# Performance work log

Hardware: AMD Instinct MI355X
Metric: run time of the kernel (lower is better)

Reference implementation:

```python
import jax, jax.numpy as jnp
import numpy as np

D = 768
H = 12
EPS = 1e-5


def layer_norm(x, g, b):
    mu = jnp.mean(x, axis=-1, keepdims=True)
    var = jnp.var(x, axis=-1, keepdims=True)
    return (x - mu) * jax.lax.rsqrt(var + EPS) * g + b


def setup_inputs() -> dict:
    key = jax.random.key(0)
    ks = jax.random.split(key, 12)
    d, h = D, H
    x = jax.random.normal(ks[0], (4, 1024, d), dtype=jnp.float32)
    # attention projections (per-head dim is full d, per the module)
    s_qkv = (6.0 / (d + d * h)) ** 0.5  # xavier-like scale
    Wq = jax.random.uniform(ks[1], (d, d * h), jnp.float32, -s_qkv, s_qkv)
    Wk = jax.random.uniform(ks[2], (d, d * h), jnp.float32, -s_qkv, s_qkv)
    Wv = jax.random.uniform(ks[3], (d, d * h), jnp.float32, -s_qkv, s_qkv)
    Wu = jax.random.uniform(ks[4], (d * h, d), jnp.float32, -s_qkv, s_qkv)
    bu = jnp.zeros((d,), jnp.float32)
    # MLP
    s1 = (6.0 / (d + 4 * d)) ** 0.5
    W1 = jax.random.uniform(ks[5], (d, 4 * d), jnp.float32, -s1, s1)
    b1 = jax.random.normal(ks[6], (4 * d,), jnp.float32) * 1e-6
    W2 = jax.random.uniform(ks[7], (4 * d, d), jnp.float32, -s1, s1)
    b2 = jax.random.normal(ks[8], (d,), jnp.float32) * 1e-6
    ln1_g = jnp.ones((d,), jnp.float32)
    ln1_b = jnp.zeros((d,), jnp.float32)
    ln2_g = jnp.ones((d,), jnp.float32)
    ln2_b = jnp.zeros((d,), jnp.float32)
    return dict(x=x, Wq=Wq, Wk=Wk, Wv=Wv, Wu=Wu, bu=bu,
                ln1_g=ln1_g, ln1_b=ln1_b, ln2_g=ln2_g, ln2_b=ln2_b,
                W1=W1, b1=b1, W2=W2, b2=b2)


def reference(x, Wq, Wk, Wv, Wu, bu, ln1_g, ln1_b, ln2_g, ln2_b, W1, b1, W2, b2):
    b, n, d = x.shape
    h = H
    # --- pre-LN attention block ---
    res = x
    y = layer_norm(x, ln1_g, ln1_b)
    qs = (y @ Wq).reshape(b, n, h, d)  # per-head dim = d (module quirk)
    ks = (y @ Wk).reshape(b, n, h, d)
    vs = (y @ Wv).reshape(b, n, h, d)
    scores = jnp.einsum('bihd,bjhd->bhij', qs, ks) / (d ** 0.5)
    w = jax.nn.softmax(scores, axis=-1)
    att = jnp.einsum('bhij,bjhd->bihd', w, vs).reshape(b, n, h * d)
    y = att @ Wu + bu
    x = y + res
    # --- pre-LN MLP block (dropout is identity at inference) ---
    res = x
    y = layer_norm(x, ln2_g, ln2_b)
    y = jax.nn.relu(y @ W1 + b1)
    y = y @ W2 + b2
    return y + res
```

## Files before the change

kernel.cpp:

```cpp
#include <hip/hip_runtime.h>
#include <cstdint>
#include <cmath>


typedef __bf16 bf16_t;
typedef __bf16 bf16x8 __attribute__((ext_vector_type(8)));
typedef __bf16 bf16x4 __attribute__((ext_vector_type(4)));
typedef float floatx4 __attribute__((ext_vector_type(4)));

#define DMODEL 768
#define NHEAD  12
#define SEQ    1024
#define NBATCH 4
#define ROWS   (NBATCH*SEQ)
#define DH     (DMODEL*NHEAD)
#define DFF    (4*DMODEL)

__device__ __forceinline__ void gload16(const bf16_t* g, bf16_t* l)
{
  __builtin_amdgcn_global_load_lds(
      (const __attribute__((address_space(1))) void*)g,
      (__attribute__((address_space(3))) void*)l,
      16, 0, 0);
}

template<bool BIAS, bool RES, bool RELU, int OMODE>
__global__ __launch_bounds__(256)
void gemm_v8(const bf16_t* __restrict__ A, const bf16_t* __restrict__ BT,
             void* __restrict__ Cv, int K, int lda, int ldb, int ldc,
             int bdiv, long sa_hi, long sa_lo, long sb_hi, long sb_lo,
             long sc_hi, long sc_lo,
             const float* __restrict__ bias, const float* __restrict__ res,
             int ldres, float alpha)
{
  __shared__ __align__(16) bf16_t As[128*64];
  __shared__ __align__(16) bf16_t Bs[128*64];

  const long nwg  = (long)gridDim.x * gridDim.y * gridDim.z;
  const long orig = blockIdx.x + (long)gridDim.x * (blockIdx.y + (long)gridDim.y * blockIdx.z);
  const long q8 = nwg >> 3, r8 = nwg & 7;
  const long xcd = orig & 7, loc = orig >> 3;
  const long swz = (xcd < r8 ? xcd*(q8+1) : r8*(q8+1) + (xcd - r8)*q8) + loc;
  const int  bix = (int)(swz % (long)gridDim.x);
  const long rem = swz / (long)gridDim.x;
  const int  biy = (int)(rem % (long)gridDim.y);
  const int  biz = (int)(rem / (long)gridDim.y);

  const int tid  = threadIdx.x;
  const int wave = tid >> 6;
  const int lane = tid & 63;
  const int r    = lane & 15;
  const int q    = lane >> 4;

  A  += (long)(biz / bdiv) * sa_hi + (long)(biz % bdiv) * sa_lo;
  BT += (long)(biz / bdiv) * sb_hi + (long)(biz % bdiv) * sb_lo;
  const long coff = (long)(biz / bdiv) * sc_hi + (long)(biz % bdiv) * sc_lo;

  const int bm = biy * 128;
  const int bn = bix * 128;
  const int wm = (wave & 1) * 64;
  const int wn = (wave >> 1) * 64;
// ... 30 lines not shown
      for (int t = 0; t < 4; ++t) {
        afrag[t] = *(const bf16x8*)(As + p*4096 + (am + t)*512 + lane*8);
        bfrag[t] = *(const bf16x8*)(Bs + p*4096 + (bb + t)*512 + lane*8);
      }
#pragma unroll
      for (int mt = 0; mt < 4; ++mt)
#pragma unroll
        for (int nt = 0; nt < 4; ++nt)
          acc[mt][nt] = __builtin_amdgcn_mfma_f32_16x16x32_bf16(
              afrag[mt], bfrag[nt], acc[mt][nt], 0, 0, 0);
    }
    __syncthreads();
  }

  const int row0 = bm + wm + q*4;
  const int col0 = bn + wn + r;
#pragma unroll
  for (int nt = 0; nt < 4; ++nt) {
    const int col = col0 + nt*16;
    float bv = 0.f;
    if (BIAS) bv = bias[col];
#pragma unroll
    for (int mt = 0; mt < 4; ++mt) {
#pragma unroll
      for (int e = 0; e < 4; ++e) {
        const int rowi = row0 + mt*16 + e;
        float v = acc[mt][nt][e] * alpha;
        if (BIAS) v += bv;
        if (RELU) v = fmaxf(v, 0.f);
        if (RES)  v += res[(long)rowi * ldres + col];
        const long idx = coff + (long)rowi * ldc + col;
        if (OMODE == 0)      ((bf16_t*)Cv)[idx] = (bf16_t)v;
        else if (OMODE == 1) ((float*)Cv)[idx] = v;
        else                 ((float*)Cv)[idx] += v;
      }
    }
  }
}

__global__ void tr_f2b_v8(const float* __restrict__ in, bf16_t* __restrict__ out,
                          int ldi, int ldo)
{
  __shared__ bf16_t tile[32][34];
  const int c0 = blockIdx.x * 32, r0 = blockIdx.y * 32;
  const int tx = threadIdx.x, ty = threadIdx.y;
#pragma unroll
  for (int i = 0; i < 4; ++i)
    tile[ty + 8*i][tx] = (bf16_t)in[(long)(r0 + ty + 8*i) * ldi + c0 + tx];
  __syncthreads();
#pragma unroll
  for (int i = 0; i < 4; ++i)
    out[(long)(c0 + ty + 8*i) * ldo + r0 + tx] = tile[tx][ty + 8*i];
}

__global__ void tr_b_v8(const bf16_t* __restrict__ in, bf16_t* __restrict__ out,
                        int ldi, int ldo, int bdiv,
                        long si_hi, long si_lo, long so_hi, long so_lo)
{
  __shared__ bf16_t tile[32][34];
  const int z = blockIdx.z;
  in  += (long)(z / bdiv) * si_hi + (long)(z % bdiv) * si_lo;
  out += (long)(z / bdiv) * so_hi + (long)(z % bdiv) * so_lo;
  const int c0 = blockIdx.x * 32, r0 = blockIdx.y * 32;
  const int tx = threadIdx.x, ty = threadIdx.y;
#pragma unroll
  for (int i = 0; i < 4; ++i)
    tile[ty + 8*i][tx] = in[(long)(r0 + ty + 8*i) * ldi + c0 + tx];
  __syncthreads();
#pragma unroll
  for (int i = 0; i < 4; ++i)
    out[(long)(c0 + ty + 8*i) * ldo + r0 + tx] = tile[tx][ty + 8*i];
}

__global__ void tr_wh_v8(const float* __restrict__ Wq, const float* __restrict__ Wk,
                         const float* __restrict__ Wv, const float* __restrict__ Wu,
                         bf16_t* __restrict__ WhT, bf16_t* __restrict__ WuTh, int h)
{
  __shared__ bf16_t tile[32][34];
  const int z = blockIdx.z;
  const float* in; bf16_t* out; int ldi;
  if (z < 3) {
    const float* W = (z == 0) ? Wq : (z == 1) ? Wk : Wv;
    in  = W + (long)h * DMODEL;
    ldi = DH;
    out = WhT + (long)z * DMODEL * DMODEL;
  } else {
    in  = Wu + (long)h * DMODEL * DMODEL;
    ldi = DMODEL;
    out = WuTh;
  }
  const int c0 = blockIdx.x * 32, r0 = blockIdx.y * 32;
  const int tx = threadIdx.x, ty = threadIdx.y;
#pragma unroll
  for (int i = 0; i < 4; ++i)
    tile[ty + 8*i][tx] = (bf16_t)in[(long)(r0 + ty + 8*i) * ldi + c0 + tx];
  __syncthreads();
#pragma unroll
  for (int i = 0; i < 4; ++i)
    out[(long)(c0 + ty + 8*i) * DMODEL + r0 + tx] = tile[tx][ty + 8*i];
}

__global__ void cast3_v8(const float* __restrict__ a, const float* __restrict__ b,
                         const float* __restrict__ c,
                         bf16_t* __restrict__ oa, bf16_t* __restrict__ ob,
                         bf16_t* __restrict__ oc)
{
  const float* src = (blockIdx.z == 0) ? a : (blockIdx.z == 1) ? b : c;
  bf16_t* dst      = (blockIdx.z == 0) ? oa : (blockIdx.z == 1) ? ob : oc;
  const long i = ((long)blockIdx.x * 256 + threadIdx.x) * 4;
  float4 v = *(const float4*)(src + i);
  bf16x4 o;
  o[0] = (bf16_t)v.x; o[1] = (bf16_t)v.y; o[2] = (bf16_t)v.z; o[3] = (bf16_t)v.w;
  *(bf16x4*)(dst + i) = o;
}

__global__ void cast1_v8(const float* __restrict__ src, bf16_t* __restrict__ dst)
{
  const long i = ((long)blockIdx.x * 256 + threadIdx.x) * 4;
  float4 v = *(const float4*)(src + i);
  bf16x4 o;
  o[0] = (bf16_t)v.x; o[1] = (bf16_t)v.y; o[2] = (bf16_t)v.z; o[3] = (bf16_t)v.w;
  *(bf16x4*)(dst + i) = o;
}

__global__ void ln_v8(const float* __restrict__ x, const float* __restrict__ g,
                      const float* __restrict__ b, bf16_t* __restrict__ y)
{
  const long row = blockIdx.x;
  const int tid = threadIdx.x;
  const float* xr = x + row * DMODEL;
  float v0 = xr[tid], v1 = xr[tid + 256], v2 = xr[tid + 512];
  float s  = v0 + v1 + v2;
  float ss = v0*v0 + v1*v1 + v2*v2;
  for (int o = 32; o; o >>= 1) { s += __shfl_down(s, o); ss += __shfl_down(ss, o); }
  __shared__ float rs[4], rss[4];
  const int wave = tid >> 6, lane = tid & 63;
  if (lane == 0) { rs[wave] = s; rss[wave] = ss; }
  __syncthreads();
  s  = rs[0] + rs[1] + rs[2] + rs[3];
  ss = rss[0] + rss[1] + rss[2] + rss[3];
  const float inv = 1.0f / (float)DMODEL;
  const float mean = s * inv;
  const float var  = ss * inv - mean * mean;
  const float rstd = rsqrtf(var + 1e-5f);
  bf16_t* yr = y + row * DMODEL;
  yr[tid]       = (bf16_t)(((v0 - mean) * rstd) * g[tid]       + b[tid]);
  yr[tid + 256] = (bf16_t)(((v1 - mean) * rstd) * g[tid + 256] + b[tid + 256]);
  yr[tid + 512] = (bf16_t)(((v2 - mean) * rstd) * g[tid + 512] + b[tid + 512]);
}

__global__ void softmax_v8(bf16_t* __restrict__ S)
{
  const long row = blockIdx.x;
  const int tid = threadIdx.x;
  bf16_t* p = S + row * SEQ + tid * 4;
  bf16x4 v = *(const bf16x4*)p;
  float f0 = (float)v[0], f1 = (float)v[1], f2 = (float)v[2], f3 = (float)v[3];
  float m = fmaxf(fmaxf(f0, f1), fmaxf(f2, f3));
  for (int o = 32; o; o >>= 1) m = fmaxf(m, __shfl_down(m, o));
  __shared__ float rm[4], rsum[4];
  const int wave = tid >> 6, lane = tid & 63;
  if (lane == 0) rm[wave] = m;
  __syncthreads();
  m = fmaxf(fmaxf(rm[0], rm[1]), fmaxf(rm[2], rm[3]));
  float e0 = __expf(f0 - m), e1 = __expf(f1 - m), e2 = __expf(f2 - m), e3 = __expf(f3 - m);
  float s = e0 + e1 + e2 + e3;
  for (int o = 32; o; o >>= 1) s += __shfl_down(s, o);
  if (lane == 0) rsum[wave] = s;
  __syncthreads();
  s = rsum[0] + rsum[1] + rsum[2] + rsum[3];
  const float invs = 1.0f / s;
  bf16x4 o4;
  o4[0] = (bf16_t)(e0 * invs); o4[1] = (bf16_t)(e1 * invs);
  o4[2] = (bf16_t)(e2 * invs); o4[3] = (bf16_t)(e3 * invs);
  *(bf16x4*)p = o4;
}

__global__ void finalize_v8(const float* __restrict__ acc, const float* __restrict__ add,
                            const float* __restrict__ bias, float* __restrict__ o)
{
  const long i = (long)blockIdx.x * 256 + threadIdx.x;
  const int c = (int)(i % DMODEL);
  o[i] = acc[i] + bias[c] + add[i];
}

template<int NP>
__global__ void reduce_v8(const float* __restrict__ p, const float* __restrict__ add,
                          const float* __restrict__ bias, float* __restrict__ o,
                          long plane)
{
  const long i = ((long)blockIdx.x * 256 + threadIdx.x) * 4;
  float4 s = *(const float4*)(p + i);
#pragma unroll
  for (int n = 1; n < NP; ++n) {
    float4 v = *(const float4*)(p + i + (long)n * plane);
    s.x += v.x; s.y += v.y; s.z += v.z; s.w += v.w;
  }
  const int c = (int)(i % DMODEL);
  float4 bv = *(const float4*)(bias + c);
  float4 av = *(const float4*)(add + i);
  float4 r;
  r.x = s.x + bv.x + av.x; r.y = s.y + bv.y + av.y;
  r.z = s.z + bv.z + av.z; r.w = s.w + bv.w + av.w;
  *(float4*)(o + i) = r;
}

extern "C" void kernel_launch(void* const* d_in, const int* in_sizes, int n_in,
                              void* d_out, int out_size, void* d_ws, size_t ws_size,
                              hipStream_t stream)
{
  (void)in_sizes; (void)n_in; (void)out_size;
  const float* x    = (const float*)d_in[0];
  const float* Wq   = (const float*)d_in[1];
  const float* Wk   = (const float*)d_in[2];
  const float* Wv   = (const float*)d_in[3];
  const float* Wu   = (const float*)d_in[4];
  const float* bu   = (const float*)d_in[5];
  const float* ln1g = (const float*)d_in[6];
  const float* ln1b = (const float*)d_in[7];
  const float* ln2g = (const float*)d_in[8];
  const float* ln2b = (const float*)d_in[9];
  const float* W1   = (const float*)d_in[10];
  const float* b1   = (const float*)d_in[11];
  const float* W2   = (const float*)d_in[12];
  const float* b2   = (const float*)d_in[13];
  float* out = (float*)d_out;

  char* ws = (char*)d_ws;
  size_t off = 0;
  auto alloc = [&](size_t bytes) -> void* {
    void* p = (void*)(ws + off);
    off += (bytes + 255) & ~(size_t)255;
    return p;
  };

  const float qk_alpha = 1.0f / sqrtf((float)DMODEL);
  dim3 tb(32, 8);

  const size_t SZ_W   = (size_t)DMODEL * DH * 2;
  const size_t SZ_MT  = (size_t)NHEAD * DMODEL * DMODEL * 2;
  const size_t SZ_Y   = (size_t)ROWS * DMODEL * 2;
  const size_t SZ_X2  = (size_t)ROWS * DMODEL * 4;

  if (ws_size >= (size_t)262e6) {
    bf16_t* MT   = (bf16_t*)alloc(SZ_MT);
    bf16_t* PhT  = (bf16_t*)alloc(SZ_MT);
    bf16_t* y    = (bf16_t*)alloc(SZ_Y);
    float*  x2f  = (float* )alloc(SZ_X2);
    float*  part = (float* )alloc((size_t)3 * ROWS * DMODEL * 4);
    bf16_t* S    = (bf16_t*)alloc((size_t)NBATCH * SEQ * NHEAD * SEQ * 2);
    bf16_t* Zt   = (bf16_t*)alloc((size_t)NBATCH * DMODEL * NHEAD * SEQ * 2);
    bf16_t* T2   = (bf16_t*)part;
    bf16_t* Wqb  = (bf16_t*)S;
    bf16_t* Wkb  = (bf16_t*)((char*)S + SZ_W);
    bf16_t* Wvb  = (bf16_t*)((char*)S + 2*SZ_W);
    bf16_t* WuT  = (bf16_t*)((char*)S + 3*SZ_W);
    bf16_t* W1T  = (bf16_t*)S;
    bf16_t* W2T  = (bf16_t*)((char*)S + 4718592);
    bf16_t* t    = (bf16_t*)((char*)S + 9437184);
    float*  partM= (float* )((char*)S + 34603008);
    bf16_t* y2   = (bf16_t*)Zt;

    cast3_v8<<<dim3(6912, 1, 3), 256, 0, stream>>>(Wq, Wk, Wv, Wqb, Wkb, Wvb);
    tr_f2b_v8<<<dim3(DMODEL/32, DH/32), tb, 0, stream>>>(Wu, WuT, DMODEL, DH);
    gemm_v8<false,false,false,0><<<dim3(6, 6, NHEAD), 256, 0, stream>>>(
        Wkb, Wqb, MT, DMODEL, DH, DH, DMODEL, NHEAD,
        0, DMODEL, 0, DMODEL, 0, (long)DMODEL*DMODEL, nullptr, nullptr, 0, 1.0f);
    gemm_v8<false,false,false,0><<<dim3(6, 6, NHEAD), 256, 0, stream>>>(
        WuT, Wvb, PhT, DMODEL, DH, DH, DMODEL, NHEAD,
        0, DMODEL, 0, DMODEL, 0, (long)DMODEL*DMODEL, nullptr, nullptr, 0, 1.0f);

    ln_v8<<<ROWS, 256, 0, stream>>>(x, ln1g, ln1b, y);
    for (int b0 = 0; b0 < NBATCH; b0 += 2) {
      const bf16_t* yb = y + (long)b0 * SEQ * DMODEL;
      gemm_v8<false,false,false,0><<<dim3(6, 8, 2*NHEAD), 256, 0, stream>>>(
          yb, MT, T2, DMODEL, DMODEL, DMODEL, DMODEL, NHEAD,
          (long)SEQ*DMODEL, 0, 0, (long)DMODEL*DMODEL,
          (long)NHEAD*SEQ*DMODEL, (long)SEQ*DMODEL,
          nullptr, nullptr, 0, 1.0f);
      gemm_v8<false,false,false,0><<<dim3(8, 8, 2*NHEAD), 256, 0, stream>>>(
          T2, yb, S + (long)b0*SEQ*NHEAD*SEQ, DMODEL, DMODEL, DMODEL, NHEAD*SEQ, NHEAD,
          (long)NHEAD*SEQ*DMODEL, (long)SEQ*DMODEL,
          (long)SEQ*DMODEL, 0,
          (long)SEQ*NHEAD*SEQ, (long)SEQ,
          nullptr, nullptr, 0, qk_alpha);
    }
    softmax_v8<<<NBATCH*SEQ*NHEAD, 256, 0, stream>>>(S);
    gemm_v8<false,false,false,0><<<dim3(8, 6, NBATCH*NHEAD), 256, 0, stream>>>(
        PhT, y, Zt, DMODEL, DMODEL, DMODEL, NHEAD*SEQ, NHEAD,
        0, (long)DMODEL*DMODEL, (long)SEQ*DMODEL, 0,
        (long)DMODEL*NHEAD*SEQ, (long)SEQ, nullptr, nullptr, 0, 1.0f);
    gemm_v8<false,false,false,1><<<dim3(6, 8, 12), 256, 0, stream>>>(
        S, Zt, part, NHEAD*SEQ/3, NHEAD*SEQ, NHEAD*SEQ, DMODEL, NBATCH,
        (long)(NHEAD*SEQ/3), (long)SEQ*NHEAD*SEQ,
        (long)(NHEAD*SEQ/3), (long)DMODEL*NHEAD*SEQ,
        (long)ROWS*DMODEL, (long)SEQ*DMODEL, nullptr, nullptr, 0, 1.0f);
    reduce_v8<3><<<(ROWS*DMODEL)/1024, 256, 0, stream>>>(
        part, x, bu, x2f, (long)ROWS*DMODEL);

    tr_f2b_v8<<<dim3(DFF/32, DMODEL/32), tb, 0, stream>>>(W1, W1T, DFF, DMODEL);
    tr_f2b_v8<<<dim3(DMODEL/32, DFF/32), tb, 0, stream>>>(W2, W2T, DMODEL, DFF);
    ln_v8<<<ROWS, 256, 0, stream>>>(x2f, ln2g, ln2b, y2);
    gemm_v8<true,false,true,0><<<dim3(DFF/128, ROWS/128, 1), 256, 0, stream>>>(
        y2, W1T, t, DMODEL, DMODEL, DMODEL, DFF, 1, 0,0,0,0,0,0, b1, nullptr, 0, 1.0f);
    gemm_v8<false,false,false,1><<<dim3(6, ROWS/128, 4), 256, 0, stream>>>(
        t, W2T, partM, DFF/4, DFF, DFF, DMODEL, 4,
        0, (long)(DFF/4), 0, (long)(DFF/4), 0, (long)ROWS*DMODEL,
        nullptr, nullptr, 0, 1.0f);
    reduce_v8<4><<<(ROWS*DMODEL)/1024, 256, 0, stream>>>(
        partM, x2f, b2, out, (long)ROWS*DMODEL);
  } else if (ws_size >= (size_t)112e6) {
    bf16_t* MT  = (bf16_t*)alloc(SZ_MT);
    bf16_t* PhT = (bf16_t*)alloc(SZ_MT);
    bf16_t* y   = (bf16_t*)alloc(SZ_Y);
    float*  x2f = (float* )alloc(SZ_X2);
    char*   BIG = (char*  )alloc((size_t)62914560);
    bf16_t* T_b  = (bf16_t*)(BIG);
    bf16_t* S_b  = (bf16_t*)(BIG + 18874368);
    bf16_t* Zt_b = (bf16_t*)(BIG + 44040192);
    float*  part = (float* )(BIG);
    bf16_t* Wqb = (bf16_t*)(BIG);
    bf16_t* Wkb = (bf16_t*)(BIG + SZ_W);
    bf16_t* Wvb = (bf16_t*)(BIG + 2*SZ_W);
    bf16_t* WuT = (bf16_t*)(BIG + 3*SZ_W);
    bf16_t* W1T   = (bf16_t*)(BIG);
    bf16_t* W2T   = (bf16_t*)(BIG + 4718592);
    bf16_t* t     = (bf16_t*)(BIG + 9437184);
    float*  partM = (float* )(BIG + 34603008);
    bf16_t* y2    = y;

    cast3_v8<<<dim3(6912, 1, 3), 256, 0, stream>>>(Wq, Wk, Wv, Wqb, Wkb, Wvb);
    tr_f2b_v8<<<dim3(DMODEL/32, DH/32), tb, 0, stream>>>(Wu, WuT, DMODEL, DH);
    gemm_v8<false,false,false,0><<<dim3(6, 6, NHEAD), 256, 0, stream>>>(
        Wkb, Wqb, MT, DMODEL, DH, DH, DMODEL, NHEAD,
        0, DMODEL, 0, DMODEL, 0, (long)DMODEL*DMODEL, nullptr, nullptr, 0, 1.0f);
    gemm_v8<false,false,false,0><<<dim3(6, 6, NHEAD), 256, 0, stream>>>(
        WuT, Wvb, PhT, DMODEL, DH, DH, DMODEL, NHEAD,
        0, DMODEL, 0, DMODEL, 0, (long)DMODEL*DMODEL, nullptr, nullptr, 0, 1.0f);

    ln_v8<<<ROWS, 256, 0, stream>>>(x, ln1g, ln1b, y);
    for (int b = 0; b < NBATCH; ++b) {
      const bf16_t* yb = y + (long)b * SEQ * DMODEL;
      gemm_v8<false,false,false,0><<<dim3(6, 8, NHEAD), 256, 0, stream>>>(
          yb, MT, T_b, DMODEL, DMODEL, DMODEL, DMODEL, NHEAD,
          0, 0, 0, (long)DMODEL*DMODEL, 0, (long)SEQ*DMODEL,
          nullptr, nullptr, 0, 1.0f);
      gemm_v8<false,false,false,0><<<dim3(8, 8, NHEAD), 256, 0, stream>>>(
          T_b, yb, S_b, DMODEL, DMODEL, DMODEL, NHEAD*SEQ, NHEAD,
          0, (long)SEQ*DMODEL, 0, 0, 0, (long)SEQ,
          nullptr, nullptr, 0, qk_alpha);
      softmax_v8<<<NHEAD*SEQ, 256, 0, stream>>>(S_b);
      gemm_v8<false,false,false,0><<<dim3(8, 6, NHEAD), 256, 0, stream>>>(
          PhT, yb, Zt_b, DMODEL, DMODEL, DMODEL, NHEAD*SEQ, NHEAD,
          0, (long)DMODEL*DMODEL, 0, 0, 0, (long)SEQ,
          nullptr, nullptr, 0, 1.0f);
      gemm_v8<false,false,false,1><<<dim3(6, 8, 6), 256, 0, stream>>>(
          S_b, Zt_b, part, NHEAD*SEQ/6, NHEAD*SEQ, NHEAD*SEQ, DMODEL, 6,
          0, (long)(NHEAD*SEQ/6), 0, (long)(NHEAD*SEQ/6), 0, (long)SEQ*DMODEL,
          nullptr, nullptr, 0, 1.0f);
      reduce_v8<6><<<(SEQ*DMODEL)/1024, 256, 0, stream>>>(
          part, x + (long)b*SEQ*DMODEL, bu, x2f + (long)b*SEQ*DMODEL,
          (long)SEQ*DMODEL);
    }

    tr_f2b_v8<<<dim3(DFF/32, DMODEL/32), tb, 0, stream>>>(W1, W1T, DFF, DMODEL);
    tr_f2b_v8<<<dim3(DMODEL/32, DFF/32), tb, 0, stream>>>(W2, W2T, DMODEL, DFF);
    ln_v8<<<ROWS, 256, 0, stream>>>(x2f, ln2g, ln2b, y2);
    gemm_v8<true,false,true,0><<<dim3(DFF/128, ROWS/128, 1), 256, 0, stream>>>(
        y2, W1T, t, DMODEL, DMODEL, DMODEL, DFF, 1, 0,0,0,0,0,0, b1, nullptr, 0, 1.0f);
    gemm_v8<false,false,false,1><<<dim3(6, ROWS/128, 2), 256, 0, stream>>>(
        t, W2T, partM, DFF/2, DFF, DFF, DMODEL, 2,
        0, (long)(DFF/2), 0, (long)(DFF/2), 0, (long)ROWS*DMODEL,
        nullptr, nullptr, 0, 1.0f);
    reduce_v8<2><<<(ROWS*DMODEL)/1024, 256, 0, stream>>>(
        partM, x2f, b2, out, (long)ROWS*DMODEL);
  } else if (ws_size >= (size_t)70e6) {
    bf16_t* MT  = (bf16_t*)alloc(SZ_MT);
    bf16_t* PhT = (bf16_t*)alloc(SZ_MT);
    bf16_t* y   = (bf16_t*)alloc(SZ_Y);
    char*   R   = (char*  )alloc((size_t)33554432);
    bf16_t* WAb = (bf16_t*)(R);
    bf16_t* WBb = (bf16_t*)(R + SZ_W);
    float*  x2f = (float* )(R);
    bf16_t* T_h = (bf16_t*)(R + 12582912);
    bf16_t* S_h = (bf16_t*)(R + 18874368);
    bf16_t* Z_h = (bf16_t*)(R + 27262976);
    bf16_t* W1T = (bf16_t*)(R + 12582912);
    bf16_t* W2T = (bf16_t*)(R + 17301504);
    bf16_t* t   = (bf16_t*)MT;
    bf16_t* y2  = y;

    cast1_v8<<<6912, 256, 0, stream>>>(Wq, WAb);
    cast1_v8<<<6912, 256, 0, stream>>>(Wk, WBb);
    gemm_v8<false,false,false,0><<<dim3(6, 6, NHEAD), 256, 0, stream>>>(
        WBb, WAb, MT, DMODEL, DH, DH, DMODEL, NHEAD,
        0, DMODEL, 0, DMODEL, 0, (long)DMODEL*DMODEL, nullptr, nullptr, 0, 1.0f);
    cast1_v8<<<6912, 256, 0, stream>>>(Wv, WAb);
    tr_f2b_v8<<<dim3(DMODEL/32, DH/32), tb, 0, stream>>>(Wu, WBb, DMODEL, DH);
    gemm_v8<false,false,false,0><<<dim3(6, 6, NHEAD), 256, 0, stream>>>(
        WBb, WAb, PhT, DMODEL, DH, DH, DMODEL, NHEAD,
        0, DMODEL, 0, DMODEL, 0, (long)DMODEL*DMODEL, nullptr, nullptr, 0, 1.0f);

    ln_v8<<<ROWS, 256, 0, stream>>>(x, ln1g, ln1b, y);
    for (int h = 0; h < NHEAD; ++h) {
      const bf16_t* MTh  = MT  + (long)h * DMODEL * DMODEL;
      const bf16_t* PhTh = PhT + (long)h * DMODEL * DMODEL;
      gemm_v8<false,false,false,0><<<dim3(6, ROWS/128, 1), 256, 0, stream>>>(
          y, MTh, T_h, DMODEL, DMODEL, DMODEL, DMODEL, 1,
          0,0,0,0,0,0, nullptr, nullptr, 0, 1.0f);
      gemm_v8<false,false,false,0><<<dim3(8, 8, NBATCH), 256, 0, stream>>>(
          T_h, y, S_h, DMODEL, DMODEL, DMODEL, SEQ, NBATCH,
          0, (long)SEQ*DMODEL, 0, (long)SEQ*DMODEL, 0, (long)SEQ*SEQ,
          nullptr, nullptr, 0, qk_alpha);
      softmax_v8<<<ROWS, 256, 0, stream>>>(S_h);
      gemm_v8<false,false,false,0><<<dim3(8, 6, NBATCH), 256, 0, stream>>>(
          PhTh, y, Z_h, DMODEL, DMODEL, DMODEL, SEQ, NBATCH,
          0, 0, 0, (long)SEQ*DMODEL, 0, (long)DMODEL*SEQ,
          nullptr, nullptr, 0, 1.0f);
      if (h == 0)
        gemm_v8<false,false,false,1><<<dim3(6, 8, NBATCH), 256, 0, stream>>>(
            S_h, Z_h, x2f, SEQ, SEQ, SEQ, DMODEL, NBATCH,
            0, (long)SEQ*SEQ, 0, (long)DMODEL*SEQ, 0, (long)SEQ*DMODEL,
            nullptr, nullptr, 0, 1.0f);
      else
        gemm_v8<false,false,false,2><<<dim3(6, 8, NBATCH), 256, 0, stream>>>(
            S_h, Z_h, x2f, SEQ, SEQ, SEQ, DMODEL, NBATCH,
            0, (long)SEQ*SEQ, 0, (long)DMODEL*SEQ, 0, (long)SEQ*DMODEL,
            nullptr, nullptr, 0, 1.0f);
    }
    finalize_v8<<<(ROWS*DMODEL)/256, 256, 0, stream>>>(x2f, x, bu, x2f);

    tr_f2b_v8<<<dim3(DFF/32, DMODEL/32), tb, 0, stream>>>(W1, W1T, DFF, DMODEL);
    tr_f2b_v8<<<dim3(DMODEL/32, DFF/32), tb, 0, stream>>>(W2, W2T, DMODEL, DFF);
    ln_v8<<<ROWS, 256, 0, stream>>>(x2f, ln2g, ln2b, y2);
    gemm_v8<true,false,true,0><<<dim3(DFF/128, ROWS/128, 1), 256, 0, stream>>>(
        y2, W1T, t, DMODEL, DMODEL, DMODEL, DFF, 1, 0,0,0,0,0,0, b1, nullptr, 0, 1.0f);
    gemm_v8<true,true,false,1><<<dim3(6, ROWS/128, 1), 256, 0, stream>>>(
        t, W2T, out, DFF/2, DFF, DFF, DMODEL, 1, 0,0,0,0,0,0,
        b2, x2f, DMODEL, 1.0f);
    gemm_v8<false,false,false,2><<<dim3(6, ROWS/128, 1), 256, 0, stream>>>(
        t + DFF/2, W2T + DFF/2, out, DFF/2, DFF, DFF, DMODEL, 1, 0,0,0,0,0,0,
        nullptr, nullptr, 0, 1.0f);
  } else {
    bf16_t* W1T   = (bf16_t*)alloc((size_t)DMODEL * DFF * 2);
    bf16_t* W2T   = (bf16_t*)alloc((size_t)DMODEL * DFF * 2);
    bf16_t* y     = (bf16_t*)alloc(SZ_Y);
    float*  x2f   = (float* )alloc(SZ_X2);
    char*   reg1  = (char*)alloc((size_t)3*DMODEL*DMODEL*2 + (size_t)DMODEL*DMODEL*2 + (size_t)SEQ*DMODEL*2);
    bf16_t* WhT   = (bf16_t*)reg1;
    bf16_t* WuTh  = (bf16_t*)(reg1 + (size_t)3*DMODEL*DMODEL*2);
    bf16_t* attb  = (bf16_t*)(reg1 + (size_t)4*DMODEL*DMODEL*2);
    bf16_t* y2    = (bf16_t*)reg1;
    char*   reg2  = (char*)alloc((size_t)SEQ*3*DMODEL*2 + (size_t)DMODEL*SEQ*2 + (size_t)SEQ*SEQ*2);
    bf16_t* QKVb  = (bf16_t*)reg2;
    bf16_t* Vtb   = (bf16_t*)(reg2 + (size_t)SEQ*3*DMODEL*2);
    bf16_t* Sb    = (bf16_t*)(reg2 + (size_t)SEQ*3*DMODEL*2 + (size_t)DMODEL*SEQ*2);
    bf16_t* tslab = (bf16_t*)reg2;

    tr_f2b_v8<<<dim3(DFF/32, DMODEL/32), tb, 0, stream>>>(W1, W1T, DFF, DMODEL);
    tr_f2b_v8<<<dim3(DMODEL/32, DFF/32), tb, 0, stream>>>(W2, W2T, DMODEL, DFF);
    ln_v8<<<ROWS, 256, 0, stream>>>(x, ln1g, ln1b, y);

    const int N3 = 3 * DMODEL;
    for (int h = 0; h < NHEAD; ++h) {
      tr_wh_v8<<<dim3(24, 24, 4), tb, 0, stream>>>(Wq, Wk, Wv, Wu, WhT, WuTh, h);
      for (int b = 0; b < NBATCH; ++b) {
        const bf16_t* yb = y + (size_t)b * SEQ * DMODEL;
        gemm_v8<false,false,false,0><<<dim3(N3/128, SEQ/128, 1), 256, 0, stream>>>(
            yb, WhT, QKVb, DMODEL, DMODEL, DMODEL, N3, 1, 0,0,0,0,0,0,
            nullptr, nullptr, 0, 1.0f);
        tr_b_v8<<<dim3(DMODEL/32, SEQ/32, 1), tb, 0, stream>>>(
            QKVb + 2*DMODEL, Vtb, N3, SEQ, 1, 0,0,0,0);
        gemm_v8<false,false,false,0><<<dim3(SEQ/128, SEQ/128, 1), 256, 0, stream>>>(
            QKVb, QKVb + DMODEL, Sb, DMODEL, N3, N3, SEQ, 1, 0,0,0,0,0,0,
            nullptr, nullptr, 0, qk_alpha);
        softmax_v8<<<SEQ, 256, 0, stream>>>(Sb);
        gemm_v8<false,false,false,0><<<dim3(DMODEL/128, SEQ/128, 1), 256, 0, stream>>>(
            Sb, Vtb, attb, SEQ, SEQ, SEQ, DMODEL, 1, 0,0,0,0,0,0,
            nullptr, nullptr, 0, 1.0f);
        float* x2b = x2f + (size_t)b * SEQ * DMODEL;
        if (h == 0)
          gemm_v8<false,false,false,1><<<dim3(DMODEL/128, SEQ/128, 1), 256, 0, stream>>>(
              attb, WuTh, x2b, DMODEL, DMODEL, DMODEL, DMODEL, 1, 0,0,0,0,0,0,
              nullptr, nullptr, 0, 1.0f);
        else
          gemm_v8<false,false,false,2><<<dim3(DMODEL/128, SEQ/128, 1), 256, 0, stream>>>(
              attb, WuTh, x2b, DMODEL, DMODEL, DMODEL, DMODEL, 1, 0,0,0,0,0,0,
              nullptr, nullptr, 0, 1.0f);
      }
    }
    finalize_v8<<<(ROWS*DMODEL)/256, 256, 0, stream>>>(x2f, x, bu, x2f);
    ln_v8<<<ROWS, 256, 0, stream>>>(x2f, ln2g, ln2b, y2);
    for (int kb = 0; kb < 4; ++kb) {
      gemm_v8<true,false,true,0><<<dim3(DMODEL/128, ROWS/128, 1), 256, 0, stream>>>(
          y2, W1T + (size_t)kb*DMODEL*DMODEL, tslab, DMODEL, DMODEL, DMODEL, DMODEL, 1,
          0,0,0,0,0,0, b1 + kb*DMODEL, nullptr, 0, 1.0f);
      if (kb == 0)
        gemm_v8<true,true,false,1><<<dim3(DMODEL/128, ROWS/128, 1), 256, 0, stream>>>(
            tslab, W2T + (size_t)kb*DMODEL, out, DMODEL, DMODEL, DFF, DMODEL, 1,
            0,0,0,0,0,0, b2, x2f, DMODEL, 1.0f);
      else
        gemm_v8<false,false,false,2><<<dim3(DMODEL/128, ROWS/128, 1), 256, 0, stream>>>(
            tslab, W2T + (size_t)kb*DMODEL, out, DMODEL, DMODEL, DFF, DMODEL, 1,
            0,0,0,0,0,0, nullptr, nullptr, 0, 1.0f);
    }
  }
}
```

Measured before the change: 994.3 us.

## Replace split-K partial buffers and reductions with atomic-add epilogue, merge batch loop

Adds an atomic-add output mode to the GEMM and uses it for the split-K attention output (now split 8 ways) and the MLP down-projection, with a small init kernel that pre-writes residual plus bias. This removes the partial-sum buffers and the separate reduce kernels, and lowers the workspace threshold for the fast path. The two-iteration batch loop is collapsed into single launches over all batches. Float atomics make the summation order nondeterministic and add contention on the outputs.

```diff
diff --git a/kernel.cpp b/kernel.cpp
--- a/kernel.cpp
+++ b/kernel.cpp
@@ -26,7 +26,7 @@
 
 template<bool BIAS, bool RES, bool RELU, int OMODE>
 __global__ __launch_bounds__(256)
-void gemm_v8(const bf16_t* __restrict__ A, const bf16_t* __restrict__ BT,
+void gemm_v9(const bf16_t* __restrict__ A, const bf16_t* __restrict__ BT,
              void* __restrict__ Cv, int K, int lda, int ldb, int ldc,
              int bdiv, long sa_hi, long sa_lo, long sb_hi, long sb_lo,
              long sc_hi, long sc_lo,
@@ -123,13 +123,14 @@
         const long idx = coff + (long)rowi * ldc + col;
         if (OMODE == 0)      ((bf16_t*)Cv)[idx] = (bf16_t)v;
         else if (OMODE == 1) ((float*)Cv)[idx] = v;
-        else                 ((float*)Cv)[idx] += v;
+        else if (OMODE == 2) ((float*)Cv)[idx] += v;
+        else                 unsafeAtomicAdd(&((float*)Cv)[idx], v);
       }
     }
   }
 }
 
-__global__ void tr_f2b_v8(const float* __restrict__ in, bf16_t* __restrict__ out,
+__global__ void tr_f2b_v9(const float* __restrict__ in, bf16_t* __restrict__ out,
                           int ldi, int ldo)
 {
   __shared__ bf16_t tile[32][34];
@@ -144,7 +145,7 @@
     out[(long)(c0 + ty + 8*i) * ldo + r0 + tx] = tile[tx][ty + 8*i];
 }
 
-__global__ void tr_b_v8(const bf16_t* __restrict__ in, bf16_t* __restrict__ out,
+__global__ void tr_b_v9(const bf16_t* __restrict__ in, bf16_t* __restrict__ out,
                         int ldi, int ldo, int bdiv,
                         long si_hi, long si_lo, long so_hi, long so_lo)
 {
@@ -163,7 +164,7 @@
     out[(long)(c0 + ty + 8*i) * ldo + r0 + tx] = tile[tx][ty + 8*i];
 }
 
-__global__ void tr_wh_v8(const float* __restrict__ Wq, const float* __restrict__ Wk,
+__global__ void tr_wh_v9(const float* __restrict__ Wq, const float* __restrict__ Wk,
                          const float* __restrict__ Wv, const float* __restrict__ Wu,
                          bf16_t* __restrict__ WhT, bf16_t* __restrict__ WuTh, int h)
 {
@@ -191,7 +192,7 @@
     out[(long)(c0 + ty + 8*i) * DMODEL + r0 + tx] = tile[tx][ty + 8*i];
 }
 
-__global__ void cast3_v8(const float* __restrict__ a, const float* __restrict__ b,
+__global__ void cast3_v9(const float* __restrict__ a, const float* __restrict__ b,
                          const float* __restrict__ c,
                          bf16_t* __restrict__ oa, bf16_t* __restrict__ ob,
                          bf16_t* __restrict__ oc)
@@ -205,7 +206,7 @@
   *(bf16x4*)(dst + i) = o;
 }
 
-__global__ void cast1_v8(const float* __restrict__ src, bf16_t* __restrict__ dst)
+__global__ void cast1_v9(const float* __restrict__ src, bf16_t* __restrict__ dst)
 {
   const long i = ((long)blockIdx.x * 256 + threadIdx.x) * 4;
   float4 v = *(const float4*)(src + i);
@@ -214,7 +215,7 @@
   *(bf16x4*)(dst + i) = o;
 }
 
-__global__ void ln_v8(const float* __restrict__ x, const float* __restrict__ g,
+__global__ void ln_v9(const float* __restrict__ x, const float* __restrict__ g,
                       const float* __restrict__ b, bf16_t* __restrict__ y)
 {
   const long row = blockIdx.x;
@@ -240,7 +241,7 @@
   yr[tid + 512] = (bf16_t)(((v2 - mean) * rstd) * g[tid + 512] + b[tid + 512]);
 }
 
-__global__ void softmax_v8(bf16_t* __restrict__ S)
+__global__ void softmax_v9(bf16_t* __restrict__ S)
 {
   const long row = blockIdx.x;
   const int tid = threadIdx.x;
@@ -267,7 +268,7 @@
   *(bf16x4*)p = o4;
 }
 
-__global__ void finalize_v8(const float* __restrict__ acc, const float* __restrict__ add,
+__global__ void finalize_v9(const float* __restrict__ acc, const float* __restrict__ add,
                             const float* __restrict__ bias, float* __restrict__ o)
 {
   const long i = (long)blockIdx.x * 256 + threadIdx.x;
@@ -275,8 +276,20 @@
   o[i] = acc[i] + bias[c] + add[i];
 }
 
+__global__ void initb_v9(const float* __restrict__ add, const float* __restrict__ bias,
+                         float* __restrict__ o)
+{
+  const long i = ((long)blockIdx.x * 256 + threadIdx.x) * 4;
+  const int c = (int)(i % DMODEL);
+  float4 av = *(const float4*)(add + i);
+  float4 bv = *(const float4*)(bias + c);
+  float4 r;
+  r.x = av.x + bv.x; r.y = av.y + bv.y; r.z = av.z + bv.z; r.w = av.w + bv.w;
+  *(float4*)(o + i) = r;
+}
+
 template<int NP>
-__global__ void reduce_v8(const float* __restrict__ p, const float* __restrict__ add,
+__global__ void reduce_v9(const float* __restrict__ p, const float* __restrict__ add,
                           const float* __restrict__ bias, float* __restrict__ o,
                           long plane)
 {
@@ -333,15 +346,14 @@
   const size_t SZ_Y   = (size_t)ROWS * DMODEL * 2;
   const size_t SZ_X2  = (size_t)ROWS * DMODEL * 4;
 
-  if (ws_size >= (size_t)262e6) {
+  if (ws_size >= (size_t)230e6) {
     bf16_t* MT   = (bf16_t*)alloc(SZ_MT);
     bf16_t* PhT  = (bf16_t*)alloc(SZ_MT);
     bf16_t* y    = (bf16_t*)alloc(SZ_Y);
     float*  x2f  = (float* )alloc(SZ_X2);
-    float*  part = (float* )alloc((size_t)3 * ROWS * DMODEL * 4);
     bf16_t* S    = (bf16_t*)alloc((size_t)NBATCH * SEQ * NHEAD * SEQ * 2);
     bf16_t* Zt   = (bf16_t*)alloc((size_t)NBATCH * DMODEL * NHEAD * SEQ * 2);
-    bf16_t* T2   = (bf16_t*)part;
+    bf16_t* T    = (bf16_t*)Zt;
     bf16_t* Wqb  = (bf16_t*)S;
     bf16_t* Wkb  = (bf16_t*)((char*)S + SZ_W);
     bf16_t* Wvb  = (bf16_t*)((char*)S + 2*SZ_W);
@@ -349,57 +361,48 @@
     bf16_t* W1T  = (bf16_t*)S;
     bf16_t* W2T  = (bf16_t*)((char*)S + 4718592);
     bf16_t* t    = (bf16_t*)((char*)S + 9437184);
-    float*  partM= (float* )((char*)S + 34603008);
     bf16_t* y2   = (bf16_t*)Zt;
 
-    cast3_v8<<<dim3(6912, 1, 3), 256, 0, stream>>>(Wq, Wk, Wv, Wqb, Wkb, Wvb);
-    tr_f2b_v8<<<dim3(DMODEL/32, DH/32), tb, 0, stream>>>(Wu, WuT, DMODEL, DH);
-    gemm_v8<false,false,false,0><<<dim3(6, 6, NHEAD), 256, 0, stream>>>(
+    cast3_v9<<<dim3(6912, 1, 3), 256, 0, stream>>>(Wq, Wk, Wv, Wqb, Wkb, Wvb);
+    tr_f2b_v9<<<dim3(DMODEL/32, DH/32), tb, 0, stream>>>(Wu, WuT, DMODEL, DH);
+    gemm_v9<false,false,false,0><<<dim3(6, 6, NHEAD), 256, 0, stream>>>(
         Wkb, Wqb, MT, DMODEL, DH, DH, DMODEL, NHEAD,
         0, DMODEL, 0, DMODEL, 0, (long)DMODEL*DMODEL, nullptr, nullptr, 0, 1.0f);
-    gemm_v8<false,false,false,0><<<dim3(6, 6, NHEAD), 256, 0, stream>>>(
+    gemm_v9<false,false,false,0><<<dim3(6, 6, NHEAD), 256, 0, stream>>>(
         WuT, Wvb, PhT, DMODEL, DH, DH, DMODEL, NHEAD,
         0, DMODEL, 0, DMODEL, 0, (long)DMODEL*DMODEL, nullptr, nullptr, 0, 1.0f);
 
-    ln_v8<<<ROWS, 256, 0, stream>>>(x, ln1g, ln1b, y);
-    for (int b0 = 0; b0 < NBATCH; b0 += 2) {
-      const bf16_t* yb = y + (long)b0 * SEQ * DMODEL;
-      gemm_v8<false,false,false,0><<<dim3(6, 8, 2*NHEAD), 256, 0, stream>>>(
-          yb, MT, T2, DMODEL, DMODEL, DMODEL, DMODEL, NHEAD,
-          (long)SEQ*DMODEL, 0, 0, (long)DMODEL*DMODEL,
-          (long)NHEAD*SEQ*DMODEL, (long)SEQ*DMODEL,
-          nullptr, nullptr, 0, 1.0f);
-      gemm_v8<false,false,false,0><<<dim3(8, 8, 2*NHEAD), 256, 0, stream>>>(
-          T2, yb, S + (long)b0*SEQ*NHEAD*SEQ, DMODEL, DMODEL, DMODEL, NHEAD*SEQ, NHEAD,
-          (long)NHEAD*SEQ*DMODEL, (long)SEQ*DMODEL,
-          (long)SEQ*DMODEL, 0,
-          (long)SEQ*NHEAD*SEQ, (long)SEQ,
-          nullptr, nullptr, 0, qk_alpha);
-    }
-    softmax_v8<<<NBATCH*SEQ*NHEAD, 256, 0, stream>>>(S);
-    gemm_v8<false,false,false,0><<<dim3(8, 6, NBATCH*NHEAD), 256, 0, stream>>>(
+    ln_v9<<<ROWS, 256, 0, stream>>>(x, ln1g, ln1b, y);
+    gemm_v9<false,false,false,0><<<dim3(6, 8, NBATCH*NHEAD), 256, 0, stream>>>(
+        y, MT, T, DMODEL, DMODEL, DMODEL, DMODEL, NHEAD,
+        (long)SEQ*DMODEL, 0, 0, (long)DMODEL*DMODEL,
+        (long)NHEAD*SEQ*DMODEL, (long)SEQ*DMODEL, nullptr, nullptr, 0, 1.0f);
+    gemm_v9<false,false,false,0><<<dim3(8, 8, NBATCH*NHEAD), 256, 0, stream>>>(
+        T, y, S, DMODEL, DMODEL, DMODEL, NHEAD*SEQ, NHEAD,
+        (long)NHEAD*SEQ*DMODEL, (long)SEQ*DMODEL, (long)SEQ*DMODEL, 0,
+        (long)SEQ*NHEAD*SEQ, (long)SEQ, nullptr, nullptr, 0, qk_alpha);
+    softmax_v9<<<NBATCH*SEQ*NHEAD, 256, 0, stream>>>(S);
+    gemm_v9<false,false,false,0><<<dim3(8, 6, NBATCH*NHEAD), 256, 0, stream>>>(
         PhT, y, Zt, DMODEL, DMODEL, DMODEL, NHEAD*SEQ, NHEAD,
         0, (long)DMODEL*DMODEL, (long)SEQ*DMODEL, 0,
         (long)DMODEL*NHEAD*SEQ, (long)SEQ, nullptr, nullptr, 0, 1.0f);
-    gemm_v8<false,false,false,1><<<dim3(6, 8, 12), 256, 0, stream>>>(
-        S, Zt, part, NHEAD*SEQ/3, NHEAD*SEQ, NHEAD*SEQ, DMODEL, NBATCH,
-        (long)(NHEAD*SEQ/3), (long)SEQ*NHEAD*SEQ,
-        (long)(NHEAD*SEQ/3), (long)DMODEL*NHEAD*SEQ,
-        (long)ROWS*DMODEL, (long)SEQ*DMODEL, nullptr, nullptr, 0, 1.0f);
-    reduce_v8<3><<<(ROWS*DMODEL)/1024, 256, 0, stream>>>(
-        part, x, bu, x2f, (long)ROWS*DMODEL);
-
-    tr_f2b_v8<<<dim3(DFF/32, DMODEL/32), tb, 0, stream>>>(W1, W1T, DFF, DMODEL);
-    tr_f2b_v8<<<dim3(DMODEL/32, DFF/32), tb, 0, stream>>>(W2, W2T, DMODEL, DFF);
-    ln_v8<<<ROWS, 256, 0, stream>>>(x2f, ln2g, ln2b, y2);
-    gemm_v8<true,false,true,0><<<dim3(DFF/128, ROWS/128, 1), 256, 0, stream>>>(
+    initb_v9<<<(ROWS*DMODEL)/1024, 256, 0, stream>>>(x, bu, x2f);
+    gemm_v9<false,false,false,3><<<dim3(6, 8, 32), 256, 0, stream>>>(
+        S, Zt, x2f, NHEAD*SEQ/8, NHEAD*SEQ, NHEAD*SEQ, DMODEL, NBATCH,
+        (long)(NHEAD*SEQ/8), (long)SEQ*NHEAD*SEQ,
+        (long)(NHEAD*SEQ/8), (long)DMODEL*NHEAD*SEQ,
+        0, (long)SEQ*DMODEL, nullptr, nullptr, 0, 1.0f);
+
+    ln_v9<<<ROWS, 256, 0, stream>>>(x2f, ln2g, ln2b, y2);
+    tr_f2b_v9<<<dim3(DFF/32, DMODEL/32), tb, 0, stream>>>(W1, W1T, DFF, DMODEL);
+    tr_f2b_v9<<<dim3(DMODEL/32, DFF/32), tb, 0, stream>>>(W2, W2T, DMODEL, DFF);
+    gemm_v9<true,false,true,0><<<dim3(DFF/128, ROWS/128, 1), 256, 0, stream>>>(
         y2, W1T, t, DMODEL, DMODEL, DMODEL, DFF, 1, 0,0,0,0,0,0, b1, nullptr, 0, 1.0f);
-    gemm_v8<false,false,false,1><<<dim3(6, ROWS/128, 4), 256, 0, stream>>>(
-        t, W2T, partM, DFF/4, DFF, DFF, DMODEL, 4,
-        0, (long)(DFF/4), 0, (long)(DFF/4), 0, (long)ROWS*DMODEL,
+    initb_v9<<<(ROWS*DMODEL)/1024, 256, 0, stream>>>(x2f, b2, out);
+    gemm_v9<false,false,false,3><<<dim3(6, ROWS/128, 4), 256, 0, stream>>>(
+        t, W2T, out, DFF/4, DFF, DFF, DMODEL, 4,
+        0, (long)(DFF/4), 0, (long)(DFF/4), 0, 0,
         nullptr, nullptr, 0, 1.0f);
-    reduce_v8<4><<<(ROWS*DMODEL)/1024, 256, 0, stream>>>(
-        partM, x2f, b2, out, (long)ROWS*DMODEL);
   } else if (ws_size >= (size_t)112e6) {
     bf16_t* MT  = (bf16_t*)alloc(SZ_MT);
     bf16_t* PhT = (bf16_t*)alloc(SZ_MT);
@@ -420,50 +423,50 @@
     float*  partM = (float* )(BIG + 34603008);
     bf16_t* y2    = y;
 
-    cast3_v8<<<dim3(6912, 1, 3), 256, 0, stream>>>(Wq, Wk, Wv, Wqb, Wkb, Wvb);
-    tr_f2b_v8<<<dim3(DMODEL/32, DH/32), tb, 0, stream>>>(Wu, WuT, DMODEL, DH);
-    gemm_v8<false,false,false,0><<<dim3(6, 6, NHEAD), 256, 0, stream>>>(
+    cast3_v9<<<dim3(6912, 1, 3), 256, 0, stream>>>(Wq, Wk, Wv, Wqb, Wkb, Wvb);
+    tr_f2b_v9<<<dim3(DMODEL/32, DH/32), tb, 0, stream>>>(Wu, WuT, DMODEL, DH);
+    gemm_v9<false,false,false,0><<<dim3(6, 6, NHEAD), 256, 0, stream>>>(
         Wkb, Wqb, MT, DMODEL, DH, DH, DMODEL, NHEAD,
         0, DMODEL, 0, DMODEL, 0, (long)DMODEL*DMODEL, nullptr, nullptr, 0, 1.0f);
-    gemm_v8<false,false,false,0><<<dim3(6, 6, NHEAD), 256, 0, stream>>>(
+    gemm_v9<false,false,false,0><<<dim3(6, 6, NHEAD), 256, 0, stream>>>(
         WuT, Wvb, PhT, DMODEL, DH, DH, DMODEL, NHEAD,
         0, DMODEL, 0, DMODEL, 0, (long)DMODEL*DMODEL, nullptr, nullptr, 0, 1.0f);
 
-    ln_v8<<<ROWS, 256, 0, stream>>>(x, ln1g, ln1b, y);
+    ln_v9<<<ROWS, 256, 0, stream>>>(x, ln1g, ln1b, y);
     for (int b = 0; b < NBATCH; ++b) {
       const bf16_t* yb = y + (long)b * SEQ * DMODEL;
-      gemm_v8<false,false,false,0><<<dim3(6, 8, NHEAD), 256, 0, stream>>>(
+      gemm_v9<false,false,false,0><<<dim3(6, 8, NHEAD), 256, 0, stream>>>(
           yb, MT, T_b, DMODEL, DMODEL, DMODEL, DMODEL, NHEAD,
           0, 0, 0, (long)DMODEL*DMODEL, 0, (long)SEQ*DMODEL,
           nullptr, nullptr, 0, 1.0f);
-      gemm_v8<false,false,false,0><<<dim3(8, 8, NHEAD), 256, 0, stream>>>(
+      gemm_v9<false,false,false,0><<<dim3(8, 8, NHEAD), 256, 0, stream>>>(
           T_b, yb, S_b, DMODEL, DMODEL, DMODEL, NHEAD*SEQ, NHEAD,
           0, (long)SEQ*DMODEL, 0, 0, 0, (long)SEQ,
           nullptr, nullptr, 0, qk_alpha);
-      softmax_v8<<<NHEAD*SEQ, 256, 0, stream>>>(S_b);
-      gemm_v8<false,false,false,0><<<dim3(8, 6, NHEAD), 256, 0, stream>>>(
+      softmax_v9<<<NHEAD*SEQ, 256, 0, stream>>>(S_b);
+      gemm_v9<false,false,false,0><<<dim3(8, 6, NHEAD), 256, 0, stream>>>(
           PhT, yb, Zt_b, DMODEL, DMODEL, DMODEL, NHEAD*SEQ, NHEAD,
           0, (long)DMODEL*DMODEL, 0, 0, 0, (long)SEQ,
           nullptr, nullptr, 0, 1.0f);
-      gemm_v8<false,false,false,1><<<dim3(6, 8, 6), 256, 0, stream>>>(
+      gemm_v9<false,false,false,1><<<dim3(6, 8, 6), 256, 0, stream>>>(
           S_b, Zt_b, part, NHEAD*SEQ/6, NHEAD*SEQ, NHEAD*SEQ, DMODEL, 6,
           0, (long)(NHEAD*SEQ/6), 0, (long)(NHEAD*SEQ/6), 0, (long)SEQ*DMODEL,
           nullptr, nullptr, 0, 1.0f);
-      reduce_v8<6><<<(SEQ*DMODEL)/1024, 256, 0, stream>>>(
+      reduce_v9<6><<<(SEQ*DMODEL)/1024, 256, 0, stream>>>(
           part, x + (long)b*SEQ*DMODEL, bu, x2f + (long)b*SEQ*DMODEL,
           (long)SEQ*DMODEL);
     }
 
-    tr_f2b_v8<<<dim3(DFF/32, DMODEL/32), tb, 0, stream>>>(W1, W1T, DFF, DMODEL);
-    tr_f2b_v8<<<dim3(DMODEL/32, DFF/32), tb, 0, stream>>>(W2, W2T, DMODEL, DFF);
-    ln_v8<<<ROWS, 256, 0, stream>>>(x2f, ln2g, ln2b, y2);
-    gemm_v8<true,false,true,0><<<dim3(DFF/128, ROWS/128, 1), 256, 0, stream>>>(
+    tr_f2b_v9<<<dim3(DFF/32, DMODEL/32), tb, 0, stream>>>(W1, W1T, DFF, DMODEL);
+    tr_f2b_v9<<<dim3(DMODEL/32, DFF/32), tb, 0, stream>>>(W2, W2T, DMODEL, DFF);
+    ln_v9<<<ROWS, 256, 0, stream>>>(x2f, ln2g, ln2b, y2);
+    gemm_v9<true,false,true,0><<<dim3(DFF/128, ROWS/128, 1), 256, 0, stream>>>(
         y2, W1T, t, DMODEL, DMODEL, DMODEL, DFF, 1, 0,0,0,0,0,0, b1, nullptr, 0, 1.0f);
-    gemm_v8<false,false,false,1><<<dim3(6, ROWS/128, 2), 256, 0, stream>>>(
+    gemm_v9<false,false,false,1><<<dim3(6, ROWS/128, 2), 256, 0, stream>>>(
         t, W2T, partM, DFF/2, DFF, DFF, DMODEL, 2,
         0, (long)(DFF/2), 0, (long)(DFF/2), 0, (long)ROWS*DMODEL,
         nullptr, nullptr, 0, 1.0f);
-    reduce_v8<2><<<(ROWS*DMODEL)/1024, 256, 0, stream>>>(
+    reduce_v9<2><<<(ROWS*DMODEL)/1024, 256, 0, stream>>>(
         partM, x2f, b2, out, (long)ROWS*DMODEL);
   } else if (ws_size >= (size_t)70e6) {
     bf16_t* MT  = (bf16_t*)alloc(SZ_MT);
@@ -481,55 +484,55 @@
     bf16_t* t   = (bf16_t*)MT;
     bf16_t* y2  = y;
 
-    cast1_v8<<<6912, 256, 0, stream>>>(Wq, WAb);
-    cast1_v8<<<6912, 256, 0, stream>>>(Wk, WBb);
-    gemm_v8<false,false,false,0><<<dim3(6, 6, NHEAD), 256, 0, stream>>>(
+    cast1_v9<<<6912, 256, 0, stream>>>(Wq, WAb);
+    cast1_v9<<<6912, 256, 0, stream>>>(Wk, WBb);
+    gemm_v9<false,false,false,0><<<dim3(6, 6, NHEAD), 256, 0, stream>>>(
         WBb, WAb, MT, DMODEL, DH, DH, DMODEL, NHEAD,
         0, DMODEL, 0, DMODEL, 0, (long)DMODEL*DMODEL, nullptr, nullptr, 0, 1.0f);
-    cast1_v8<<<6912, 256, 0, stream>>>(Wv, WAb);
-    tr_f2b_v8<<<dim3(DMODEL/32, DH/32), tb, 0, stream>>>(Wu, WBb, DMODEL, DH);
-    gemm_v8<false,false,false,0><<<dim3(6, 6, NHEAD), 256, 0, stream>>>(
+    cast1_v9<<<6912, 256, 0, stream>>>(Wv, WAb);
+    tr_f2b_v9<<<dim3(DMODEL/32, DH/32), tb, 0, stream>>>(Wu, WBb, DMODEL, DH);
+    gemm_v9<false,false,false,0><<<dim3(6, 6, NHEAD), 256, 0, stream>>>(
         WBb, WAb, PhT, DMODEL, DH, DH, DMODEL, NHEAD,
         0, DMODEL, 0, DMODEL, 0, (long)DMODEL*DMODEL, nullptr, nullptr, 0, 1.0f);
 
-    ln_v8<<<ROWS, 256, 0, stream>>>(x, ln1g, ln1b, y);
+    ln_v9<<<ROWS, 256, 0, stream>>>(x, ln1g, ln1b, y);
     for (int h = 0; h < NHEAD; ++h) {
       const bf16_t* MTh  = MT  + (long)h * DMODEL * DMODEL;
       const bf16_t* PhTh = PhT + (long)h * DMODEL * DMODEL;
-      gemm_v8<false,false,false,0><<<dim3(6, ROWS/128, 1), 256, 0, stream>>>(
+      gemm_v9<false,false,false,0><<<dim3(6, ROWS/128, 1), 256, 0, stream>>>(
           y, MTh, T_h, DMODEL, DMODEL, DMODEL, DMODEL, 1,
           0,0,0,0,0,0, nullptr, nullptr, 0, 1.0f);
-      gemm_v8<false,false,false,0><<<dim3(8, 8, NBATCH), 256, 0, stream>>>(
+      gemm_v9<false,false,false,0><<<dim3(8, 8, NBATCH), 256, 0, stream>>>(
           T_h, y, S_h, DMODEL, DMODEL, DMODEL, SEQ, NBATCH,
           0, (long)SEQ*DMODEL, 0, (long)SEQ*DMODEL, 0, (long)SEQ*SEQ,
           nullptr, nullptr, 0, qk_alpha);
-      softmax_v8<<<ROWS, 256, 0, stream>>>(S_h);
-      gemm_v8<false,false,false,0><<<dim3(8, 6, NBATCH), 256, 0, stream>>>(
+      softmax_v9<<<ROWS, 256, 0, stream>>>(S_h);
+      gemm_v9<false,false,false,0><<<dim3(8, 6, NBATCH), 256, 0, stream>>>(
           PhTh, y, Z_h, DMODEL, DMODEL, DMODEL, SEQ, NBATCH,
           0, 0, 0, (long)SEQ*DMODEL, 0, (long)DMODEL*SEQ,
           nullptr, nullptr, 0, 1.0f);
       if (h == 0)
-        gemm_v8<false,false,false,1><<<dim3(6, 8, NBATCH), 256, 0, stream>>>(
+        gemm_v9<false,false,false,1><<<dim3(6, 8, NBATCH), 256, 0, stream>>>(
             S_h, Z_h, x2f, SEQ, SEQ, SEQ, DMODEL, NBATCH,
             0, (long)SEQ*SEQ, 0, (long)DMODEL*SEQ, 0, (long)SEQ*DMODEL,
             nullptr, nullptr, 0, 1.0f);
       else
-        gemm_v8<false,false,false,2><<<dim3(6, 8, NBATCH), 256, 0, stream>>>(
+        gemm_v9<false,false,false,2><<<dim3(6, 8, NBATCH), 256, 0, stream>>>(
             S_h, Z_h, x2f, SEQ, SEQ, SEQ, DMODEL, NBATCH,
             0, (long)SEQ*SEQ, 0, (long)DMODEL*SEQ, 0, (long)SEQ*DMODEL,
             nullptr, nullptr, 0, 1.0f);
     }
-    finalize_v8<<<(ROWS*DMODEL)/256, 256, 0, stream>>>(x2f, x, bu, x2f);
-
-    tr_f2b_v8<<<dim3(DFF/32, DMODEL/32), tb, 0, stream>>>(W1, W1T, DFF, DMODEL);
-    tr_f2b_v8<<<dim3(DMODEL/32, DFF/32), tb, 0, stream>>>(W2, W2T, DMODEL, DFF);
-    ln_v8<<<ROWS, 256, 0, stream>>>(x2f, ln2g, ln2b, y2);
-    gemm_v8<true,false,true,0><<<dim3(DFF/128, ROWS/128, 1), 256, 0, stream>>>(
+    finalize_v9<<<(ROWS*DMODEL)/256, 256, 0, stream>>>(x2f, x, bu, x2f);
+
+    tr_f2b_v9<<<dim3(DFF/32, DMODEL/32), tb, 0, stream>>>(W1, W1T, DFF, DMODEL);
+    tr_f2b_v9<<<dim3(DMODEL/32, DFF/32), tb, 0, stream>>>(W2, W2T, DMODEL, DFF);
+    ln_v9<<<ROWS, 256, 0, stream>>>(x2f, ln2g, ln2b, y2);
+    gemm_v9<true,false,true,0><<<dim3(DFF/128, ROWS/128, 1), 256, 0, stream>>>(
         y2, W1T, t, DMODEL, DMODEL, DMODEL, DFF, 1, 0,0,0,0,0,0, b1, nullptr, 0, 1.0f);
-    gemm_v8<true,true,false,1><<<dim3(6, ROWS/128, 1), 256, 0, stream>>>(
+    gemm_v9<true,true,false,1><<<dim3(6, ROWS/128, 1), 256, 0, stream>>>(
         t, W2T, out, DFF/2, DFF, DFF, DMODEL, 1, 0,0,0,0,0,0,
         b2, x2f, DMODEL, 1.0f);
-    gemm_v8<false,false,false,2><<<dim3(6, ROWS/128, 1), 256, 0, stream>>>(
+    gemm_v9<false,false,false,2><<<dim3(6, ROWS/128, 1), 256, 0, stream>>>(
         t + DFF/2, W2T + DFF/2, out, DFF/2, DFF, DFF, DMODEL, 1, 0,0,0,0,0,0,
         nullptr, nullptr, 0, 1.0f);
   } else {
@@ -548,50 +551,50 @@
     bf16_t* Sb    = (bf16_t*)(reg2 + (size_t)SEQ*3*DMODEL*2 + (size_t)DMODEL*SEQ*2);
     bf16_t* tslab = (bf16_t*)reg2;
 
-    tr_f2b_v8<<<dim3(DFF/32, DMODEL/32), tb, 0, stream>>>(W1, W1T, DFF, DMODEL);
-    tr_f2b_v8<<<dim3(DMODEL/32, DFF/32), tb, 0, stream>>>(W2, W2T, DMODEL, DFF);
-    ln_v8<<<ROWS, 256, 0, stream>>>(x, ln1g, ln1b, y);
+    tr_f2b_v9<<<dim3(DFF/32, DMODEL/32), tb, 0, stream>>>(W1, W1T, DFF, DMODEL);
+    tr_f2b_v9<<<dim3(DMODEL/32, DFF/32), tb, 0, stream>>>(W2, W2T, DMODEL, DFF);
+    ln_v9<<<ROWS, 256, 0, stream>>>(x, ln1g, ln1b, y);
 
     const int N3 = 3 * DMODEL;
     for (int h = 0; h < NHEAD; ++h) {
-      tr_wh_v8<<<dim3(24, 24, 4), tb, 0, stream>>>(Wq, Wk, Wv, Wu, WhT, WuTh, h);
+      tr_wh_v9<<<dim3(24, 24, 4), tb, 0, stream>>>(Wq, Wk, Wv, Wu, WhT, WuTh, h);
       for (int b = 0; b < NBATCH; ++b) {
         const bf16_t* yb = y + (size_t)b * SEQ * DMODEL;
-        gemm_v8<false,false,false,0><<<dim3(N3/128, SEQ/128, 1), 256, 0, stream>>>(
+        gemm_v9<false,false,false,0><<<dim3(N3/128, SEQ/128, 1), 256, 0, stream>>>(
             yb, WhT, QKVb, DMODEL, DMODEL, DMODEL, N3, 1, 0,0,0,0,0,0,
             nullptr, nullptr, 0, 1.0f);
-        tr_b_v8<<<dim3(DMODEL/32, SEQ/32, 1), tb, 0, stream>>>(
+        tr_b_v9<<<dim3(DMODEL/32, SEQ/32, 1), tb, 0, stream>>>(
             QKVb + 2*DMODEL, Vtb, N3, SEQ, 1, 0,0,0,0);
-        gemm_v8<false,false,false,0><<<dim3(SEQ/128, SEQ/128, 1), 256, 0, stream>>>(
+        gemm_v9<false,false,false,0><<<dim3(SEQ/128, SEQ/128, 1), 256, 0, stream>>>(
             QKVb, QKVb + DMODEL, Sb, DMODEL, N3, N3, SEQ, 1, 0,0,0,0,0,0,
             nullptr, nullptr, 0, qk_alpha);
-        softmax_v8<<<SEQ, 256, 0, stream>>>(Sb);
-        gemm_v8<false,false,false,0><<<dim3(DMODEL/128, SEQ/128, 1), 256, 0, stream>>>(
+        softmax_v9<<<SEQ, 256, 0, stream>>>(Sb);
+        gemm_v9<false,false,false,0><<<dim3(DMODEL/128, SEQ/128, 1), 256, 0, stream>>>(
             Sb, Vtb, attb, SEQ, SEQ, SEQ, DMODEL, 1, 0,0,0,0,0,0,
             nullptr, nullptr, 0, 1.0f);
         float* x2b = x2f + (size_t)b * SEQ * DMODEL;
         if (h == 0)
-          gemm_v8<false,false,false,1><<<dim3(DMODEL/128, SEQ/128, 1), 256, 0, stream>>>(
+          gemm_v9<false,false,false,1><<<dim3(DMODEL/128, SEQ/128, 1), 256, 0, stream>>>(
               attb, WuTh, x2b, DMODEL, DMODEL, DMODEL, DMODEL, 1, 0,0,0,0,0,0,
               nullptr, nullptr, 0, 1.0f);
         else
-          gemm_v8<false,false,false,2><<<dim3(DMODEL/128, SEQ/128, 1), 256, 0, stream>>>(
+          gemm_v9<false,false,false,2><<<dim3(DMODEL/128, SEQ/128, 1), 256, 0, stream>>>(
               attb, WuTh, x2b, DMODEL, DMODEL, DMODEL, DMODEL, 1, 0,0,0,0,0,0,
               nullptr, nullptr, 0, 1.0f);
       }
     }
-    finalize_v8<<<(ROWS*DMODEL)/256, 256, 0, stream>>>(x2f, x, bu, x2f);
-    ln_v8<<<ROWS, 256, 0, stream>>>(x2f, ln2g, ln2b, y2);
+    finalize_v9<<<(ROWS*DMODEL)/256, 256, 0, stream>>>(x2f, x, bu, x2f);
+    ln_v9<<<ROWS, 256, 0, stream>>>(x2f, ln2g, ln2b, y2);
     for (int kb = 0; kb < 4; ++kb) {
-      gemm_v8<true,false,true,0><<<dim3(DMODEL/128, ROWS/128, 1), 256, 0, stream>>>(
+      gemm_v9<true,false,true,0><<<dim3(DMODEL/128, ROWS/128, 1), 256, 0, stream>>>(
           y2, W1T + (size_t)kb*DMODEL*DMODEL, tslab, DMODEL, DMODEL, DMODEL, DMODEL, 1,
           0,0,0,0,0,0, b1 + kb*DMODEL, nullptr, 0, 1.0f);
       if (kb == 0)
-        gemm_v8<true,true,false,1><<<dim3(DMODEL/128, ROWS/128, 1), 256, 0, stream>>>(
+        gemm_v9<true,true,false,1><<<dim3(DMODEL/128, ROWS/128, 1), 256, 0, stream>>>(
             tslab, W2T + (size_t)kb*DMODEL, out, DMODEL, DMODEL, DFF, DMODEL, 1,
             0,0,0,0,0,0, b2, x2f, DMODEL, 1.0f);
       else
-        gemm_v8<false,false,false,2><<<dim3(DMODEL/128, ROWS/128, 1), 256, 0, stream>>>(
+        gemm_v9<false,false,false,2><<<dim3(DMODEL/128, ROWS/128, 1), 256, 0, stream>>>(
             tslab, W2T + (size_t)kb*DMODEL, out, DMODEL, DMODEL, DFF, DMODEL, 1,
             0,0,0,0,0,0, nullptr, nullptr, 0, 1.0f);
     }
```

After: 958.4 us. 1.04x faster.
